# Kernel optimization log

Measured on AMD Instinct MI355X. Metric: run time of the kernel, lower is better.

## Reference

```python
import jax, jax.numpy as jnp
import numpy as np

B, T, C = 32, 1536, 768
G, Vg = 2, 160  # num_groups, vars_per_group (num_vars=320)
TEMP = 2.0


def setup_inputs() -> dict:
    key = jax.random.key(0)
    kx, kg, kw, kc = jax.random.split(key, 4)
    x = jax.random.normal(kx, (B, T, C), dtype=jnp.float32)
    # Gumbel(0,1) noise, equivalent to torch's -log(Exp(1).sample())
    gumbel = jax.random.gumbel(kg, (B, T, G, Vg), dtype=jnp.float32)
    W_proj = jax.random.normal(kw, (C, G * Vg), dtype=jnp.float32) * (1.0 / np.sqrt(C))
    b_proj = jnp.zeros((G * Vg,), dtype=jnp.float32)
    codebook = jax.random.normal(kc, (G, Vg, C), dtype=jnp.float32)
    return {"x": x, "gumbel": gumbel, "W_proj": W_proj, "b_proj": b_proj, "codebook": codebook}


def reference(x, gumbel, W_proj, b_proj, codebook):
    b, t, c = x.shape
    g, vg, _ = codebook.shape
    logits = (x @ W_proj + b_proj).reshape(b, t, g, vg)          # (B,T,G,Vg)
    probs = jax.nn.softmax((logits + gumbel) / TEMP, axis=-1)    # (B,T,G,Vg)
    codes = jnp.argmax(probs, axis=-1)                           # (B,T,G)
    # Fused codebook contraction: sum over vars AND groups in one GEMM-like einsum,
    # avoiding the naive (B,T,G,Vg,C) broadcast intermediate.
    quantized = jnp.einsum('btgv,gvc->btc', probs, codebook)     # (B,T,C)
    return quantized, codes, probs
```

## Files before the change

kernel.cpp:

```cpp
#include <hip/hip_runtime.h>
#include <hip/hip_bf16.h>
#include <stdint.h>

#define BT_TOK   49152
#define C_DIM    768
#define NVARS    320
#define VG       160
#define NGROUPS  2

__device__ __forceinline__ unsigned short bf16_rne(float f) {
    union { float f; uint32_t u; } v; v.f = f;
    uint32_t u = v.u + 0x7FFFu + ((v.u >> 16) & 1u);
    return (unsigned short)(u >> 16);
}
__device__ __forceinline__ float bf16_to_f(unsigned short h) {
    union { uint32_t u; float f; } v; v.u = ((uint32_t)h) << 16;
    return v.f;
}

typedef __attribute__((ext_vector_type(8))) short bf16x8;
typedef __attribute__((ext_vector_type(4))) float f32x4;

#define GLOBAL_AS __attribute__((address_space(1)))
#define LDS_AS    __attribute__((address_space(3)))
__device__ __forceinline__ void gl2lds16(const void* g, void* l) {
    __builtin_amdgcn_global_load_lds((const GLOBAL_AS void*)g, (LDS_AS void*)l, 16, 0, 0);
}

__global__ __launch_bounds__(256)
void split_convert(const float* __restrict__ in, unsigned short* __restrict__ hi,
                   unsigned short* __restrict__ lo, int n) {
    int i = (blockIdx.x * 256 + threadIdx.x) * 4;
    if (i >= n) return;
    float4 v = *(const float4*)(in + i);
    ushort4 h, l;
    h.x = bf16_rne(v.x); l.x = bf16_rne(v.x - bf16_to_f(h.x));
    h.y = bf16_rne(v.y); l.y = bf16_rne(v.y - bf16_to_f(h.y));
    h.z = bf16_rne(v.z); l.z = bf16_rne(v.z - bf16_to_f(h.z));
    h.w = bf16_rne(v.w); l.w = bf16_rne(v.w - bf16_to_f(h.w));
    *(ushort4*)(hi + i) = h;
    *(ushort4*)(lo + i) = l;
}

__global__ __launch_bounds__(256)
void transpose_split(const float* __restrict__ in, unsigned short* __restrict__ hi,
                     unsigned short* __restrict__ lo, int K, int N) {
    int k = blockIdx.x * 256 + threadIdx.x;
    int n = blockIdx.y;
    if (k >= K) return;
    float f = in[(size_t)k * N + n];
    unsigned short h = bf16_rne(f);
    hi[(size_t)n * K + k] = h;
    lo[(size_t)n * K + k] = bf16_rne(f - bf16_to_f(h));
}

template<int BM, int BN, int WM, int WN>
__global__ __launch_bounds__(WM*WN*64)
void gemm_split(const unsigned short* __restrict__ Ahi, const unsigned short* __restrict__ Alo,
                const unsigned short* __restrict__ Bthi, const unsigned short* __restrict__ Btlo,
                const float* __restrict__ bias, float* __restrict__ C,
                int M, int N, int K)
{
    constexpr int NW = WM * WN;
    constexpr int nIterA = (BM * 4) / 64;
    constexpr int nIterB = (BN * 4) / 64;

    __shared__ __align__(16) unsigned short sAh[BM * 32];
    __shared__ __align__(16) unsigned short sAl[BM * 32];
    __shared__ __align__(16) unsigned short sBh[BN * 32];
    __shared__ __align__(16) unsigned short sBl[BN * 32];

    const int tid  = threadIdx.x;
    const int lane = tid & 63;
    const int wid  = tid >> 6;
    const int wm   = wid % WM;
    const int wn   = wid / WM;
    const int m0   = blockIdx.y * BM;
    const int n0   = blockIdx.x * BN;

    const int r15 = lane & 15;
    const int q   = lane >> 4;

    f32x4 acc[4][4];
#pragma unroll
    for (int i = 0; i < 4; ++i)
#pragma unroll
        for (int j = 0; j < 4; ++j) {
            f32x4 z = {0.f, 0.f, 0.f, 0.f};
            acc[i][j] = z;
        }

    for (int k0 = 0; k0 < K; k0 += 32) {
        for (int i = wid; i < nIterA; i += NW) {
            int slot = i * 64 + lane;
            int row  = slot >> 2, cs = slot & 3;
            int c    = cs ^ ((row >> 1) & 3);
            size_t goff = (size_t)(m0 + row) * K + k0 + c * 8;
            gl2lds16(Ahi + goff, (char*)sAh + i * 1024);
            gl2lds16(Alo + goff, (char*)sAl + i * 1024);
        }
        for (int i = wid; i < nIterB; i += NW) {
            int slot = i * 64 + lane;
            int row  = slot >> 2, cs = slot & 3;
            int c    = cs ^ ((row >> 1) & 3);
            size_t goff = (size_t)(n0 + row) * K + k0 + c * 8;
            gl2lds16(Bthi + goff, (char*)sBh + i * 1024);
            gl2lds16(Btlo + goff, (char*)sBl + i * 1024);
        }
        __syncthreads();

        bf16x8 ah[4], al[4], bh[4], bl[4];
#pragma unroll
        for (int mi = 0; mi < 4; ++mi) {
            int row = wm * 64 + mi * 16 + r15;
            int off = row * 32 + ((q ^ ((row >> 1) & 3)) * 8);
            ah[mi] = *(const bf16x8*)&sAh[off];
            al[mi] = *(const bf16x8*)&sAl[off];
        }
#pragma unroll
        for (int ni = 0; ni < 4; ++ni) {
            int row = wn * 64 + ni * 16 + r15;
            int off = row * 32 + ((q ^ ((row >> 1) & 3)) * 8);
            bh[ni] = *(const bf16x8*)&sBh[off];
            bl[ni] = *(const bf16x8*)&sBl[off];
        }

#pragma unroll
        for (int mi = 0; mi < 4; ++mi)
#pragma unroll
            for (int ni = 0; ni < 4; ++ni) {
                acc[mi][ni] = __builtin_amdgcn_mfma_f32_16x16x32_bf16(ah[mi], bh[ni], acc[mi][ni], 0, 0, 0);
                acc[mi][ni] = __builtin_amdgcn_mfma_f32_16x16x32_bf16(ah[mi], bl[ni], acc[mi][ni], 0, 0, 0);
                acc[mi][ni] = __builtin_amdgcn_mfma_f32_16x16x32_bf16(al[mi], bh[ni], acc[mi][ni], 0, 0, 0);
            }
        __syncthreads();
    }

#pragma unroll
    for (int ni = 0; ni < 4; ++ni) {
        int col = n0 + wn * 64 + ni * 16 + r15;
        float bv = bias ? bias[col] : 0.f;
#pragma unroll
        for (int mi = 0; mi < 4; ++mi) {
            int rbase = m0 + wm * 64 + mi * 16 + q * 4;
#pragma unroll
            for (int rr = 0; rr < 4; ++rr)
                C[(size_t)(rbase + rr) * N + col] = acc[mi][ni][rr] + bv;
        }
    }
}

__global__ __launch_bounds__(256)
void gumbel_softmax_kernel(float* __restrict__ logits_probs,
                           const float* __restrict__ gumbel,
                           float* __restrict__ codes,
                           unsigned short* __restrict__ phi,
                           unsigned short* __restrict__ plo)
{
    const int wid  = (int)((blockIdx.x * (size_t)blockDim.x + threadIdx.x) >> 6);
    const int lane = threadIdx.x & 63;
    if (wid >= BT_TOK * NGROUPS) return;

    float* base        = logits_probs + (size_t)wid * VG;
    const float* gbase = gumbel       + (size_t)wid * VG;

    const float NEG = -3.402823466e+38f;
    float y[3];
    float mx = NEG;
#pragma unroll
    for (int i = 0; i < 3; ++i) {
        int v = lane + i * 64;
        float val = NEG;
        if (v < VG) val = (base[v] + gbase[v]) * 0.5f;
        y[i] = val;
        mx = fmaxf(mx, val);
    }
#pragma unroll
    for (int off = 32; off > 0; off >>= 1)
        mx = fmaxf(mx, __shfl_xor(mx, off, 64));

    float e[3];
    float s = 0.f;
#pragma unroll
    for (int i = 0; i < 3; ++i) {
        int v = lane + i * 64;
        e[i] = (v < VG) ? expf(y[i] - mx) : 0.f;
        s += e[i];
    }
#pragma unroll
    for (int off = 32; off > 0; off >>= 1)
        s += __shfl_xor(s, off, 64);
    const float inv = 1.0f / s;

#pragma unroll
    for (int i = 0; i < 3; ++i) {
        int v = lane + i * 64;
        if (v < VG) {
            float p = e[i] * inv;
            base[v] = p;
            if (phi) {
                unsigned short h = bf16_rne(p);
                phi[(size_t)wid * VG + v] = h;
                plo[(size_t)wid * VG + v] = bf16_rne(p - bf16_to_f(h));
            }
        }
    }

    float bv = y[0];
    int   bi = lane;
#pragma unroll
    for (int i = 1; i < 3; ++i) {
        int v = lane + i * 64;
        if (v < VG && y[i] > bv) { bv = y[i]; bi = v; }
    }
#pragma unroll
    for (int off = 32; off > 0; off >>= 1) {
        float ov = __shfl_xor(bv, off, 64);
        int   oi = __shfl_xor(bi, off, 64);
        if (ov > bv || (ov == bv && oi < bi)) { bv = ov; bi = oi; }
    }
    if (lane == 0) codes[wid] = (float)bi;
}

__global__ __launch_bounds__(256)
void sgemm64(const float* __restrict__ A, const float* __restrict__ B,
             const float* __restrict__ bias, float* __restrict__ C,
             int M, int N, int K)
{
    const int tid = threadIdx.x;
    const int n0  = blockIdx.x * 64;
    const int m0  = blockIdx.y * 64;

    __shared__ float As[16][64 + 4];
    __shared__ float Bs[16][64];

    const int a_row = tid >> 2;
    const int a_k   = (tid & 3) * 4;
    const int b_row = tid >> 4;
    const int b_col = (tid & 15) * 4;
    const int tx = tid & 15;
    const int ty = tid >> 4;

    float acc[4][4] = {};

    for (int k0 = 0; k0 < K; k0 += 16) {
        float4 av = *(const float4*)(A + (size_t)(m0 + a_row) * K + k0 + a_k);
        float4 bv = *(const float4*)(B + (size_t)(k0 + b_row) * N + n0 + b_col);
        __syncthreads();
        As[a_k + 0][a_row] = av.x;
        As[a_k + 1][a_row] = av.y;
        As[a_k + 2][a_row] = av.z;
        As[a_k + 3][a_row] = av.w;
        *(float4*)&Bs[b_row][b_col] = bv;
        __syncthreads();
#pragma unroll
        for (int k = 0; k < 16; ++k) {
            float4 a4 = *(const float4*)&As[k][ty * 4];
            float4 b4 = *(const float4*)&Bs[k][tx * 4];
            const float a[4] = {a4.x, a4.y, a4.z, a4.w};
            const float b[4] = {b4.x, b4.y, b4.z, b4.w};
#pragma unroll
            for (int r = 0; r < 4; ++r)
#pragma unroll
                for (int c = 0; c < 4; ++c)
                    acc[r][c] = fmaf(a[r], b[c], acc[r][c]);
        }
    }

    float4 bs = make_float4(0.f, 0.f, 0.f, 0.f);
    if (bias) bs = *(const float4*)(bias + n0 + tx * 4);
#pragma unroll
    for (int r = 0; r < 4; ++r) {
        float4 o;
        o.x = acc[r][0] + bs.x;
        o.y = acc[r][1] + bs.y;
        o.z = acc[r][2] + bs.z;
        o.w = acc[r][3] + bs.w;
        *(float4*)(C + (size_t)(m0 + ty * 4 + r) * N + n0 + tx * 4) = o;
    }
}

extern "C" void kernel_launch(void* const* d_in, const int* in_sizes, int n_in,
                              void* d_out, int out_size, void* d_ws, size_t ws_size,
                              hipStream_t stream) {
    const float* x        = (const float*)d_in[0];
    const float* gumbel   = (const float*)d_in[1];
    const float* W_proj   = (const float*)d_in[2];
    const float* b_proj   = (const float*)d_in[3];
    const float* codebook = (const float*)d_in[4];

    float* quantized = (float*)d_out;
    float* codes     = quantized + (size_t)BT_TOK * C_DIM;
    float* probs     = codes + (size_t)BT_TOK * NGROUPS;

    const size_t SZ_X  = (size_t)BT_TOK * C_DIM * 2;
    const size_t SZ_P  = (size_t)BT_TOK * NVARS * 2;
    const size_t SZ_W  = (size_t)C_DIM * NVARS * 2;
    const size_t need  = 2 * SZ_X + 2 * SZ_P + 4 * SZ_W;

    if (ws_size >= need) {
        char* ws = (char*)d_ws;
        unsigned short* xhi  = (unsigned short*)(ws);
        unsigned short* xlo  = (unsigned short*)(ws + SZ_X);
        unsigned short* wthi = (unsigned short*)(ws + 2 * SZ_X);
        unsigned short* wtlo = (unsigned short*)(ws + 2 * SZ_X + SZ_W);
        unsigned short* cthi = (unsigned short*)(ws + 2 * SZ_X + 2 * SZ_W);
        unsigned short* ctlo = (unsigned short*)(ws + 2 * SZ_X + 3 * SZ_W);
        unsigned short* phi  = (unsigned short*)(ws + 2 * SZ_X + 4 * SZ_W);
        unsigned short* plo  = (unsigned short*)(ws + 2 * SZ_X + 4 * SZ_W + SZ_P);

        split_convert<<<(BT_TOK * C_DIM / 4 + 255) / 256, 256, 0, stream>>>(
            x, xhi, xlo, BT_TOK * C_DIM);
        transpose_split<<<dim3((C_DIM + 255) / 256, NVARS), 256, 0, stream>>>(
            W_proj, wthi, wtlo, C_DIM, NVARS);
        transpose_split<<<dim3((NVARS + 255) / 256, C_DIM), 256, 0, stream>>>(
            codebook, cthi, ctlo, NVARS, C_DIM);

        gemm_split<64, 320, 1, 5><<<dim3(1, BT_TOK / 64), 320, 0, stream>>>(
            xhi, xlo, wthi, wtlo, b_proj, probs, BT_TOK, NVARS, C_DIM);

        gumbel_softmax_kernel<<<BT_TOK * NGROUPS / 4, 256, 0, stream>>>(
            probs, gumbel, codes, phi, plo);

        gemm_split<64, 384, 1, 6><<<dim3(C_DIM / 384, BT_TOK / 64), 384, 0, stream>>>(
            phi, plo, cthi, ctlo, nullptr, quantized, BT_TOK, C_DIM, NVARS);
    } else {
        dim3 g1(NVARS / 64, BT_TOK / 64);
        sgemm64<<<g1, 256, 0, stream>>>(x, W_proj, b_proj, probs, BT_TOK, NVARS, C_DIM);
        gumbel_softmax_kernel<<<BT_TOK * NGROUPS / 4, 256, 0, stream>>>(
            probs, gumbel, codes, nullptr, nullptr);
        dim3 g2(C_DIM / 64, BT_TOK / 64);
        sgemm64<<<g2, 256, 0, stream>>>(probs, codebook, nullptr, quantized, BT_TOK, C_DIM, NVARS);
    }
}
```

Baseline: 670.2 us.

## Double-buffer LDS staging in split-bf16 GEMMs and enlarge second GEMM tile

```diff
diff --git a/kernel.cpp b/kernel.cpp
--- a/kernel.cpp
+++ b/kernel.cpp
@@ -55,20 +55,20 @@
 }
 
 template<int BM, int BN, int WM, int WN>
-__global__ __launch_bounds__(WM*WN*64)
-void gemm_split(const unsigned short* __restrict__ Ahi, const unsigned short* __restrict__ Alo,
-                const unsigned short* __restrict__ Bthi, const unsigned short* __restrict__ Btlo,
-                const float* __restrict__ bias, float* __restrict__ C,
-                int M, int N, int K)
+__global__ __launch_bounds__(WM*WN*64, (WM*WN+3)/4)
+void gemm_split_db(const unsigned short* __restrict__ Ahi, const unsigned short* __restrict__ Alo,
+                   const unsigned short* __restrict__ Bthi, const unsigned short* __restrict__ Btlo,
+                   const float* __restrict__ bias, float* __restrict__ C,
+                   int M, int N, int K)
 {
     constexpr int NW = WM * WN;
     constexpr int nIterA = (BM * 4) / 64;
     constexpr int nIterB = (BN * 4) / 64;
-
-    __shared__ __align__(16) unsigned short sAh[BM * 32];
-    __shared__ __align__(16) unsigned short sAl[BM * 32];
-    __shared__ __align__(16) unsigned short sBh[BN * 32];
-    __shared__ __align__(16) unsigned short sBl[BN * 32];
+    constexpr int ABYTES = BM * 32 * 2;
+    constexpr int BBYTES = BN * 32 * 2;
+    constexpr int BUFBYTES = 2 * ABYTES + 2 * BBYTES;
+
+    extern __shared__ __align__(16) char smem[];
 
     const int tid  = threadIdx.x;
     const int lane = tid & 63;
@@ -90,24 +90,38 @@
             acc[i][j] = z;
         }
 
-    for (int k0 = 0; k0 < K; k0 += 32) {
+    auto stage = [&](int buf, int k0) {
+        char* base = smem + buf * BUFBYTES;
         for (int i = wid; i < nIterA; i += NW) {
             int slot = i * 64 + lane;
             int row  = slot >> 2, cs = slot & 3;
             int c    = cs ^ ((row >> 1) & 3);
             size_t goff = (size_t)(m0 + row) * K + k0 + c * 8;
-            gl2lds16(Ahi + goff, (char*)sAh + i * 1024);
-            gl2lds16(Alo + goff, (char*)sAl + i * 1024);
+            gl2lds16(Ahi + goff, base + i * 1024);
+            gl2lds16(Alo + goff, base + ABYTES + i * 1024);
         }
         for (int i = wid; i < nIterB; i += NW) {
             int slot = i * 64 + lane;
             int row  = slot >> 2, cs = slot & 3;
             int c    = cs ^ ((row >> 1) & 3);
             size_t goff = (size_t)(n0 + row) * K + k0 + c * 8;
-            gl2lds16(Bthi + goff, (char*)sBh + i * 1024);
-            gl2lds16(Btlo + goff, (char*)sBl + i * 1024);
-        }
-        __syncthreads();
+            gl2lds16(Bthi + goff, base + 2 * ABYTES + i * 1024);
+            gl2lds16(Btlo + goff, base + 2 * ABYTES + BBYTES + i * 1024);
+        }
+    };
+
+    const int NT = K / 32;
+    stage(0, 0);
+    __syncthreads();
+
+    int cur = 0;
+    for (int t = 0; t < NT; ++t) {
+        if (t + 1 < NT) stage(cur ^ 1, (t + 1) * 32);
+
+        const unsigned short* sAh = (const unsigned short*)(smem + cur * BUFBYTES);
+        const unsigned short* sAl = (const unsigned short*)(smem + cur * BUFBYTES + ABYTES);
+        const unsigned short* sBh = (const unsigned short*)(smem + cur * BUFBYTES + 2 * ABYTES);
+        const unsigned short* sBl = (const unsigned short*)(smem + cur * BUFBYTES + 2 * ABYTES + BBYTES);
 
         bf16x8 ah[4], al[4], bh[4], bl[4];
 #pragma unroll
@@ -133,7 +147,9 @@
                 acc[mi][ni] = __builtin_amdgcn_mfma_f32_16x16x32_bf16(ah[mi], bl[ni], acc[mi][ni], 0, 0, 0);
                 acc[mi][ni] = __builtin_amdgcn_mfma_f32_16x16x32_bf16(al[mi], bh[ni], acc[mi][ni], 0, 0, 0);
             }
+
         __syncthreads();
+        cur ^= 1;
     }
 
 #pragma unroll
@@ -298,7 +314,19 @@
     const size_t SZ_W  = (size_t)C_DIM * NVARS * 2;
     const size_t need  = 2 * SZ_X + 2 * SZ_P + 4 * SZ_W;
 
+    constexpr int SH1 = 2 * (2 * (64 * 32 * 2)  + 2 * (320 * 32 * 2));
+    constexpr int SH2 = 2 * (2 * (128 * 32 * 2) + 2 * (384 * 32 * 2));
+
     if (ws_size >= need) {
+        static bool s_init = false;
+        if (!s_init) {
+            hipFuncSetAttribute(reinterpret_cast<const void*>(&gemm_split_db<64, 320, 1, 5>),
+                                hipFuncAttributeMaxDynamicSharedMemorySize, SH1);
+            hipFuncSetAttribute(reinterpret_cast<const void*>(&gemm_split_db<128, 384, 2, 6>),
+                                hipFuncAttributeMaxDynamicSharedMemorySize, SH2);
+            s_init = true;
+        }
+
         char* ws = (char*)d_ws;
         unsigned short* xhi  = (unsigned short*)(ws);
         unsigned short* xlo  = (unsigned short*)(ws + SZ_X);
@@ -316,13 +344,13 @@
         transpose_split<<<dim3((NVARS + 255) / 256, C_DIM), 256, 0, stream>>>(
             codebook, cthi, ctlo, NVARS, C_DIM);
 
-        gemm_split<64, 320, 1, 5><<<dim3(1, BT_TOK / 64), 320, 0, stream>>>(
+        gemm_split_db<64, 320, 1, 5><<<dim3(1, BT_TOK / 64), 320, SH1, stream>>>(
             xhi, xlo, wthi, wtlo, b_proj, probs, BT_TOK, NVARS, C_DIM);
 
         gumbel_softmax_kernel<<<BT_TOK * NGROUPS / 4, 256, 0, stream>>>(
             probs, gumbel, codes, phi, plo);
 
-        gemm_split<64, 384, 1, 6><<<dim3(C_DIM / 384, BT_TOK / 64), 384, 0, stream>>>(
+        gemm_split_db<128, 384, 2, 6><<<dim3(C_DIM / 384, BT_TOK / 128), 768, SH2, stream>>>(
             phi, plo, cthi, ctlo, nullptr, quantized, BT_TOK, C_DIM, NVARS);
     } else {
         dim3 g1(NVARS / 64, BT_TOK / 64);
```

New measurement: 578.6 us. -13.7%, faster.
